# Optimization experiments

Measured on AMD Instinct MI355X. Metric: run time of the kernel, lower is better.

Reference implementation:

```python
import jax, jax.numpy as jnp
import numpy as np

N_A = 3
N_CLS = 80
IGNORE_THRE = 0.6
EPS = 1e-7


def _pairwise_iou_cxcywh(a, b):
    # a: [..., M, 4], b: [..., N, 4] in (cx, cy, w, h) -> IoU [..., M, N]
    a_xy, a_wh = a[..., :, None, :2], a[..., :, None, 2:4]
    b_xy, b_wh = b[..., None, :, :2], b[..., None, :, 2:4]
    tl = jnp.maximum(a_xy - a_wh * 0.5, b_xy - b_wh * 0.5)
    br = jnp.minimum(a_xy + a_wh * 0.5, b_xy + b_wh * 0.5)
    inter = jnp.prod(jnp.clip(br - tl, 0.0), axis=-1)
    area_a = a_wh[..., 0] * a_wh[..., 1]
    area_b = b_wh[..., 0] * b_wh[..., 1]
    return inter / jnp.maximum(area_a + area_b - inter, 1e-16)


def _bce(p, t):
    p = jnp.clip(p, EPS, 1.0 - EPS)
    return -(t * jnp.log(p) + (1.0 - t) * jnp.log(1.0 - p))


def _yolo_loss(raw, labels, anchors_all, anchor_indices, img_size):
    nB = raw.shape[0]
    nG = raw.shape[2]
    nCH = 5 + N_CLS
    K = labels.shape[1]
    sg = jax.lax.stop_gradient

    # decode raw: (B, A*CH, G, G) -> (B, A, G, G, CH)
    raw = jnp.transpose(raw.reshape(nB, N_A, nCH, nG, nG), (0, 1, 3, 4, 2))
    xy_offset = jax.nn.sigmoid(raw[..., 0:2])            # (B,A,G,G,2)
    wh_scale = raw[..., 2:4]                             # (B,A,G,G,2)
    conf = jax.nn.sigmoid(raw[..., 4])                   # (B,A,G,G)
    classes = jax.nn.sigmoid(raw[..., 5:])               # (B,A,G,G,ncls)

    anchors = anchors_all[anchor_indices]                # (3,2), pixels
    g = jnp.arange(nG, dtype=raw.dtype)
    xs = g[None, None, None, :]
    ys = g[None, None, :, None]

    # detached decoded predictions, normalized to [0,1]
    px = (sg(xy_offset[..., 0]) + xs) / nG
    py = (sg(xy_offset[..., 1]) + ys) / nG
    pw = jnp.minimum(jnp.exp(sg(wh_scale[..., 0])) * anchors[:, 0][None, :, None, None] / img_size, 1.0)
    ph = jnp.minimum(jnp.exp(sg(wh_scale[..., 1])) * anchors[:, 1][None, :, None, None] / img_size, 1.0)
    pred_boxes = jnp.stack([px, py, pw, ph], axis=-1).reshape(nB, -1, 4)  # (B, A*G*G, 4)

    # labels: (B, K, 5) = [cls, xc, yc, w, h]; targets are constants
    labels = sg(labels)
    nlabel = jnp.sum(jnp.sum(labels, axis=2) > 0, axis=1)                 # (B,)
    valid_k = jnp.arange(K)[None, :] < nlabel[:, None]                    # (B,K)
    tcls = labels[..., 0].astype(jnp.int32)
    tx = labels[..., 1] * nG
    ty = labels[..., 2] * nG
    tw = labels[..., 3]
    th = labels[..., 4]
    ti = tx.astype(jnp.int32)
    tj = ty.astype(jnp.int32)

    # anchor matching on centered (0,0,w,h) boxes against all 9 anchors
    anch00 = jnp.concatenate([jnp.zeros_like(anchors_all), anchors_all / img_size], axis=1)  # (9,4)
    gt00 = jnp.stack([jnp.zeros_like(tw), jnp.zeros_like(tw), tw, th], axis=-1)              # (B,K,4)
    a_ious = _pairwise_iou_cxcywh(gt00, anch00[None])                                        # (B,K,9)
    best_n_all = jnp.argmax(a_ious, axis=-1)                                                 # (B,K)
    valid_anchor = jnp.any(best_n_all[..., None] == anchor_indices[None, None, :], axis=-1)
    valid = valid_k & valid_anchor                                                           # (B,K)
    best_n = best_n_all % N_A

    # ignore mask: preds whose best IoU against any (valid) gt exceeds threshold
    gt_boxes = jnp.stack([tx / nG, ty / nG, tw, th], axis=-1) * valid_k[..., None].astype(raw.dtype)
    pred_ious = _pairwise_iou_cxcywh(pred_boxes, gt_boxes)               # (B, A*G*G, K)
    ignore = (jnp.max(pred_ious, axis=-1) > IGNORE_THRE).reshape(nB, N_A, nG, nG)
    penalty_mask = ~ignore

    # scatter gt assignments; invalid rows dropped via OOB batch index
    b_idx = jnp.broadcast_to(jnp.arange(nB)[:, None], (nB, K))
    b_s = jnp.where(valid, b_idx, nB)

    obj_mask = jnp.zeros((nB, N_A, nG, nG), dtype=bool).at[b_s, best_n, tj, ti].set(True, mode='drop')
    penalty_mask = penalty_mask.at[b_s, best_n, tj, ti].set(True, mode='drop')

    naw = anchors / img_size                                             # (3,2)
    tgt_vals = jnp.stack([
        tx - jnp.floor(tx),
        ty - jnp.floor(ty),
        jnp.log(tw / naw[best_n, 0] + 1e-16),
        jnp.log(th / naw[best_n, 1] + 1e-16),
    ], axis=-1)                                                          # (B,K,4)
    target4 = jnp.zeros((nB, N_A, nG, nG, 4), raw.dtype).at[b_s, best_n, tj, ti].set(tgt_vals, mode='drop')
    tgt_scale = jnp.zeros((nB, N_A, nG, nG), raw.dtype).at[b_s, best_n, tj, ti].set(
        jnp.sqrt(2.0 - tw * th), mode='drop')
    tcls_oh = jnp.zeros((nB, N_A, nG, nG, N_CLS), raw.dtype).at[b_s, best_n, tj, ti, tcls].set(1.0, mode='drop')

    obj_f = obj_mask.astype(raw.dtype)
    pen_f = penalty_mask.astype(raw.dtype)
    w2 = tgt_scale * tgt_scale                                           # (B,A,G,G)

    loss_xy = jnp.sum(obj_f[..., None] * w2[..., None] * _bce(xy_offset, target4[..., 0:2]))
    loss_wh = jnp.sum(obj_f[..., None] * w2[..., None] * jnp.square(wh_scale - target4[..., 2:4]))
    loss_obj = jnp.sum(pen_f * _bce(conf, obj_f))
    loss_cls = jnp.sum(obj_f[..., None] * _bce(classes, tcls_oh))
    return loss_xy + 0.5 * loss_wh + loss_obj + loss_cls


def setup_inputs() -> dict:
    key = jax.random.key(0)
    k1, k2, k3, k4 = jax.random.split(key, 4)
    nB, K, nG = 16, 50, 76
    raw = jax.random.normal(k1, (nB, N_A * (5 + N_CLS), nG, nG), jnp.float32) * 0.5
    cls = jax.random.randint(k2, (nB, K), 0, N_CLS).astype(jnp.float32)
    xy = jax.random.uniform(k3, (nB, K, 2), jnp.float32, 0.02, 0.98)
    wh = jax.random.uniform(k4, (nB, K, 2), jnp.float32, 0.02, 0.4)
    labels = jnp.concatenate([cls[..., None], xy, wh], axis=-1)
    # make per-image label counts < K (rows of zeros are "no label")
    labels = labels * (jnp.arange(K) < 40).astype(jnp.float32)[None, :, None]
    anchors_all = jnp.array([[10, 13], [16, 30], [33, 23], [30, 61], [62, 45],
                             [59, 119], [116, 90], [156, 198], [373, 326]], jnp.float32)
    anchor_indices = jnp.array([0, 1, 2], jnp.int32)
    return {"raw": raw, "labels": labels, "anchors_all": anchors_all,
            "anchor_indices": anchor_indices, "img_size": 608}


def reference(raw, labels, anchors_all, anchor_indices, img_size):
    return _yolo_loss(raw, labels, anchors_all, anchor_indices, img_size)
```

## Files before the change

### kernel.cpp

```cpp
#include <hip/hip_runtime.h>
#include <math.h>

#define NB   16
#define KL   50
#define NG   76
#define NA   3
#define NCLS 80
#define NCH  85
#define GG   (NG*NG)
#define CELLS (NA*GG)
#define LOSS_BX ((CELLS + 255) / 256)
#define NPART (LOSS_BX * NB)

__device__ __forceinline__ float softplusf(float x) {
    float t = __expf(-fabsf(x));
    return fmaxf(x, 0.0f) + __logf(1.0f + t);
}

__global__ __launch_bounds__(64) void yolo_prep(
    const float* __restrict__ labels,
    const float* __restrict__ anchors_all,
    const int*   __restrict__ anchor_indices,
    const int*   __restrict__ img_size_p,
    int*    __restrict__ meta_ws,
    float4* __restrict__ box_ws,
    float*  __restrict__ c_ws,
    float*  __restrict__ tgt_ws,
    float*  __restrict__ w2_ws,
    int*    __restrict__ tc_ws)
{
    const int b = blockIdx.x;
    const int k = threadIdx.x;
    const float img = (float)img_size_p[0];

    int has = 0;
    float cls = 0.f, tx = 0.f, ty = 0.f, tw = 0.f, th = 0.f;
    if (k < KL) {
        const float* L = labels + ((size_t)b * KL + k) * 5;
        cls = L[0];
        float lx = L[1], ly = L[2];
        tw = L[3]; th = L[4];
        has = ((cls + lx + ly + tw + th) > 0.0f) ? 1 : 0;
        tx = lx * (float)NG;
        ty = ly * (float)NG;
    }
    unsigned long long bal = __ballot(has);
    int nlabel = __popcll(bal);
    if (k >= KL) return;

    int valid_k = (k < nlabel) ? 1 : 0;

    float best = -1.0f; int bestn = 0;
    float area_t = tw * th;
    for (int n = 0; n < 9; ++n) {
        float aw = anchors_all[2 * n + 0] / img;
        float ah = anchors_all[2 * n + 1] / img;
        float inter = fmaxf(fminf(tw, aw), 0.0f) * fmaxf(fminf(th, ah), 0.0f);
        float iou = inter / fmaxf(area_t + aw * ah - inter, 1e-16f);
        if (iou > best) { best = iou; bestn = n; }
    }
    int va = 0;
    for (int t = 0; t < 3; ++t) va |= (bestn == anchor_indices[t]) ? 1 : 0;
    int bn = bestn % NA;
    int ti = (int)tx, tj = (int)ty;
    int valid = valid_k && va && (ti >= 0) && (ti < NG) && (tj >= 0) && (tj < NG);

    const size_t idx = (size_t)b * KL + k;
    meta_ws[idx] = valid ? (bn * GG + tj * NG + ti) : -1;

    float vkf = valid_k ? 1.0f : 0.0f;
    float gx = (tx / (float)NG) * vkf;
    float gy = (ty / (float)NG) * vkf;
    float gw = tw * vkf;
    float gh = th * vkf;
    box_ws[idx] = make_float4(gx - 0.5f * gw, gy - 0.5f * gh,
                              gx + 0.5f * gw, gy + 0.5f * gh);
    c_ws[idx] = 0.375f * (gw * gh);

    float naw = anchors_all[anchor_indices[bn] * 2 + 0] / img;
    float nah = anchors_all[anchor_indices[bn] * 2 + 1] / img;
    float* T = tgt_ws + idx * 4;
    T[0] = tx - floorf(tx);
    T[1] = ty - floorf(ty);
    T[2] = logf(tw / naw + 1e-16f);
    T[3] = logf(th / nah + 1e-16f);
    w2_ws[idx] = 2.0f - tw * th;
    tc_ws[idx] = (int)cls;
}

__global__ __launch_bounds__(256) void yolo_loss(
    const float* __restrict__ raw,
    const float* __restrict__ anchors_all,
    const int*   __restrict__ anchor_indices,
    const int*   __restrict__ img_size_p,
    const int*   __restrict__ meta_ws,
    const float4* __restrict__ box_ws,
    const float* __restrict__ c_ws,
    const float* __restrict__ tgt_ws,
    const float* __restrict__ w2_ws,
    const int*   __restrict__ tc_ws,
    float* __restrict__ partials)
{
    const int b = blockIdx.y;
    const int c0 = blockIdx.x * 256 + threadIdx.x;
    const bool live = c0 < CELLS;
    const int c = live ? c0 : 0;

    const int a = c / GG;
    const int r = c - a * GG;
    const int j = r / NG;
    const int i = r - j * NG;
    const float img = (float)img_size_p[0];
    const float* R = raw + ((size_t)(b * NA + a) * NCH) * GG + r;

    float rx = R[0],        ry = R[GG];
    float rw = R[2 * GG],   rh = R[3 * GG];
    float rc = R[4 * GG];

    float sx = __builtin_amdgcn_rcpf(1.0f + __expf(-rx));
    float sy = __builtin_amdgcn_rcpf(1.0f + __expf(-ry));

    int ai = anchor_indices[a];
    float aw = anchors_all[2 * ai + 0] / img;
    float ah = anchors_all[2 * ai + 1] / img;

    float px = (sx + (float)i) * (1.0f / (float)NG);
    float py = (sy + (float)j) * (1.0f / (float)NG);
    float pw = fminf(__expf(rw) * aw, 1.0f);
    float ph = fminf(__expf(rh) * ah, 1.0f);

    float tA = 0.375f * (pw * ph);
    float ax0 = px - 0.5f * pw, ax1 = px + 0.5f * pw;
    float ay0 = py - 0.5f * ph, ay1 = py + 0.5f * ph;

    const float4* __restrict__ Gbox  = box_ws  + (size_t)b * KL;
    const float*  __restrict__ Gc    = c_ws    + (size_t)b * KL;
    const int*    __restrict__ Gmeta = meta_ws + (size_t)b * KL;

    float margin = -1.0f;
    int kobj = -1;
    #pragma unroll 10
    for (int k = 0; k < KL; ++k) {
        float4 g = Gbox[k];
        float cB = Gc[k];
        int   mk = Gmeta[k];
        float iw = fminf(ax1, g.z) - fmaxf(ax0, g.x);
        float ih = fminf(ay1, g.w) - fmaxf(ay0, g.y);
        float inter = fmaxf(iw, 0.0f) * fmaxf(ih, 0.0f);
        margin = fmaxf(margin, inter - cB);
        kobj = (mk == c) ? k : kobj;
    }
    bool ignore = margin > tA;
    bool obj = (kobj >= 0) && live;

    float loss = 0.0f;
    if (obj || !ignore)
        loss = softplusf(rc) - (obj ? rc : 0.0f);

    if (obj) {
        size_t kb = (size_t)b * KL + kobj;
        float w2 = w2_ws[kb];
        float t0 = tgt_ws[4 * kb + 0], t1 = tgt_ws[4 * kb + 1];
        float t2 = tgt_ws[4 * kb + 2], t3 = tgt_ws[4 * kb + 3];
        loss += w2 * ((softplusf(rx) - t0 * rx) + (softplusf(ry) - t1 * ry));
        float dw = rw - t2, dh = rh - t3;
        loss += 0.5f * w2 * (dw * dw + dh * dh);
        int tc = tc_ws[kb];
        float cl = 0.0f;
        #pragma unroll 8
        for (int cc = 0; cc < NCLS; ++cc) {
            float z = R[(5 + cc) * GG];
            cl += softplusf(z);
            if (cc == tc) cl -= z;
        }
        loss += cl;
    }
    if (!live) loss = 0.0f;

    for (int off = 32; off > 0; off >>= 1)
        loss += __shfl_down(loss, off, 64);
    __shared__ float s_red[4];
    if ((threadIdx.x & 63) == 0) s_red[threadIdx.x >> 6] = loss;
    __syncthreads();
    if (threadIdx.x == 0)
        partials[(size_t)blockIdx.y * gridDim.x + blockIdx.x] =
            s_red[0] + s_red[1] + s_red[2] + s_red[3];
}

__global__ __launch_bounds__(256) void yolo_finalize(
    const float* __restrict__ partials, float* __restrict__ out)
{
    float s = 0.0f;
    for (int i = threadIdx.x; i < NPART; i += 256) s += partials[i];
    for (int off = 32; off > 0; off >>= 1)
        s += __shfl_down(s, off, 64);
    __shared__ float red[4];
    if ((threadIdx.x & 63) == 0) red[threadIdx.x >> 6] = s;
    __syncthreads();
    if (threadIdx.x == 0) out[0] = red[0] + red[1] + red[2] + red[3];
}

extern "C" void kernel_launch(void* const* d_in, const int* in_sizes, int n_in,
                              void* d_out, int out_size, void* d_ws, size_t ws_size,
                              hipStream_t stream) {
    const float* raw            = (const float*)d_in[0];
    const float* labels         = (const float*)d_in[1];
    const float* anchors_all    = (const float*)d_in[2];
    const int*   anchor_indices = (const int*)d_in[3];
    const int*   img_size_p     = (const int*)d_in[4];
    float* out = (float*)d_out;

    char* ws = (char*)d_ws;
    float4* box_ws  = (float4*)ws;  ws += sizeof(float4) * NB * KL;
    float*  tgt_ws  = (float*)ws;   ws += sizeof(float)  * NB * KL * 4;
    float*  c_ws    = (float*)ws;   ws += sizeof(float)  * NB * KL;
    float*  w2_ws   = (float*)ws;   ws += sizeof(float)  * NB * KL;
    int*    meta_ws = (int*)ws;     ws += sizeof(int)    * NB * KL;
    int*    tc_ws   = (int*)ws;     ws += sizeof(int)    * NB * KL;
    float*  partials= (float*)ws;   ws += sizeof(float)  * NPART;

    yolo_prep<<<NB, 64, 0, stream>>>(labels, anchors_all, anchor_indices,
                                     img_size_p, meta_ws, box_ws, c_ws,
                                     tgt_ws, w2_ws, tc_ws);

    dim3 grid(LOSS_BX, NB);
    yolo_loss<<<grid, 256, 0, stream>>>(raw, anchors_all, anchor_indices,
                                        img_size_p, meta_ws, box_ws, c_ws,
                                        tgt_ws, w2_ws, tc_ws, partials);

    yolo_finalize<<<1, 256, 0, stream>>>(partials, out);
}
```

Baseline: 146.2 us.

## Fuse label preprocessing into loss kernel using shared memory per block

Removes the separate prep kernel launch. Each loss block now recomputes the per-image label targets, boxes and match indices in its first wavefront and keeps them in LDS, so the inner 50-label loop reads shared memory instead of global workspace. This saves a launch and a global round trip, but every block repeats the small label computation and the other wavefronts wait at a barrier. Divisions by the image size become reciprocal multiplies, and logf becomes __logf.

```diff
diff --git a/kernel.cpp b/kernel.cpp
--- a/kernel.cpp
+++ b/kernel.cpp
@@ -17,91 +17,81 @@
     return fmaxf(x, 0.0f) + __logf(1.0f + t);
 }
 
-__global__ __launch_bounds__(64) void yolo_prep(
+__global__ __launch_bounds__(256) void yolo_fused(
+    const float* __restrict__ raw,
     const float* __restrict__ labels,
     const float* __restrict__ anchors_all,
     const int*   __restrict__ anchor_indices,
     const int*   __restrict__ img_size_p,
-    int*    __restrict__ meta_ws,
-    float4* __restrict__ box_ws,
-    float*  __restrict__ c_ws,
-    float*  __restrict__ tgt_ws,
-    float*  __restrict__ w2_ws,
-    int*    __restrict__ tc_ws)
-{
-    const int b = blockIdx.x;
-    const int k = threadIdx.x;
-    const float img = (float)img_size_p[0];
-
-    int has = 0;
-    float cls = 0.f, tx = 0.f, ty = 0.f, tw = 0.f, th = 0.f;
-    if (k < KL) {
-        const float* L = labels + ((size_t)b * KL + k) * 5;
-        cls = L[0];
-        float lx = L[1], ly = L[2];
-        tw = L[3]; th = L[4];
-        has = ((cls + lx + ly + tw + th) > 0.0f) ? 1 : 0;
-        tx = lx * (float)NG;
-        ty = ly * (float)NG;
-    }
-    unsigned long long bal = __ballot(has);
-    int nlabel = __popcll(bal);
-    if (k >= KL) return;
-
-    int valid_k = (k < nlabel) ? 1 : 0;
-
-    float best = -1.0f; int bestn = 0;
-    float area_t = tw * th;
-    for (int n = 0; n < 9; ++n) {
-        float aw = anchors_all[2 * n + 0] / img;
-        float ah = anchors_all[2 * n + 1] / img;
-        float inter = fmaxf(fminf(tw, aw), 0.0f) * fmaxf(fminf(th, ah), 0.0f);
-        float iou = inter / fmaxf(area_t + aw * ah - inter, 1e-16f);
-        if (iou > best) { best = iou; bestn = n; }
-    }
-    int va = 0;
-    for (int t = 0; t < 3; ++t) va |= (bestn == anchor_indices[t]) ? 1 : 0;
-    int bn = bestn % NA;
-    int ti = (int)tx, tj = (int)ty;
-    int valid = valid_k && va && (ti >= 0) && (ti < NG) && (tj >= 0) && (tj < NG);
-
-    const size_t idx = (size_t)b * KL + k;
-    meta_ws[idx] = valid ? (bn * GG + tj * NG + ti) : -1;
-
-    float vkf = valid_k ? 1.0f : 0.0f;
-    float gx = (tx / (float)NG) * vkf;
-    float gy = (ty / (float)NG) * vkf;
-    float gw = tw * vkf;
-    float gh = th * vkf;
-    box_ws[idx] = make_float4(gx - 0.5f * gw, gy - 0.5f * gh,
-                              gx + 0.5f * gw, gy + 0.5f * gh);
-    c_ws[idx] = 0.375f * (gw * gh);
-
-    float naw = anchors_all[anchor_indices[bn] * 2 + 0] / img;
-    float nah = anchors_all[anchor_indices[bn] * 2 + 1] / img;
-    float* T = tgt_ws + idx * 4;
-    T[0] = tx - floorf(tx);
-    T[1] = ty - floorf(ty);
-    T[2] = logf(tw / naw + 1e-16f);
-    T[3] = logf(th / nah + 1e-16f);
-    w2_ws[idx] = 2.0f - tw * th;
-    tc_ws[idx] = (int)cls;
-}
-
-__global__ __launch_bounds__(256) void yolo_loss(
-    const float* __restrict__ raw,
-    const float* __restrict__ anchors_all,
-    const int*   __restrict__ anchor_indices,
-    const int*   __restrict__ img_size_p,
-    const int*   __restrict__ meta_ws,
-    const float4* __restrict__ box_ws,
-    const float* __restrict__ c_ws,
-    const float* __restrict__ tgt_ws,
-    const float* __restrict__ w2_ws,
-    const int*   __restrict__ tc_ws,
     float* __restrict__ partials)
 {
     const int b = blockIdx.y;
+
+    __shared__ float4 s_box[KL];
+    __shared__ float  s_c[KL];
+    __shared__ int    s_meta[KL];
+    __shared__ float  s_tgt[KL][4];
+    __shared__ float  s_w2[KL];
+    __shared__ int    s_tc[KL];
+    __shared__ float  s_red[4];
+
+    const float img = (float)img_size_p[0];
+    const float inv_img = __builtin_amdgcn_rcpf(img);
+
+    if (threadIdx.x < 64) {
+        const int k = threadIdx.x;
+        int has = 0;
+        float cls = 0.f, tx = 0.f, ty = 0.f, tw = 0.f, th = 0.f;
+        if (k < KL) {
+            const float* L = labels + ((size_t)b * KL + k) * 5;
+            cls = L[0];
+            tw = L[3]; th = L[4];
+            has = ((cls + L[1] + L[2] + tw + th) > 0.0f) ? 1 : 0;
+            tx = L[1] * (float)NG;
+            ty = L[2] * (float)NG;
+        }
+        unsigned long long bal = __ballot(has);
+        int nlabel = __popcll(bal);
+
+        if (k < KL) {
+            int valid_k = (k < nlabel) ? 1 : 0;
+
+            float best = -1.0f; int bestn = 0;
+            float area_t = tw * th;
+            for (int n = 0; n < 9; ++n) {
+                float aw = anchors_all[2 * n + 0] * inv_img;
+                float ah = anchors_all[2 * n + 1] * inv_img;
+                float inter = fmaxf(fminf(tw, aw), 0.0f) * fmaxf(fminf(th, ah), 0.0f);
+                float iou = inter / fmaxf(area_t + aw * ah - inter, 1e-16f);
+                if (iou > best) { best = iou; bestn = n; }
+            }
+            int va = 0;
+            for (int t = 0; t < 3; ++t) va |= (bestn == anchor_indices[t]) ? 1 : 0;
+            int bn = bestn % NA;
+            int ti = (int)tx, tj = (int)ty;
+            int valid = valid_k && va && (ti >= 0) && (ti < NG) && (tj >= 0) && (tj < NG);
+            s_meta[k] = valid ? (bn * GG + tj * NG + ti) : -1;
+
+            float vkf = valid_k ? 1.0f : 0.0f;
+            float gx = tx * (1.0f / (float)NG) * vkf;
+            float gy = ty * (1.0f / (float)NG) * vkf;
+            float gw = tw * vkf, gh = th * vkf;
+            s_box[k] = make_float4(gx - 0.5f * gw, gy - 0.5f * gh,
+                                   gx + 0.5f * gw, gy + 0.5f * gh);
+            s_c[k] = 0.375f * (gw * gh);
+
+            float naw = anchors_all[anchor_indices[bn] * 2 + 0] * inv_img;
+            float nah = anchors_all[anchor_indices[bn] * 2 + 1] * inv_img;
+            s_tgt[k][0] = tx - floorf(tx);
+            s_tgt[k][1] = ty - floorf(ty);
+            s_tgt[k][2] = __logf(tw / naw + 1e-16f);
+            s_tgt[k][3] = __logf(th / nah + 1e-16f);
+            s_w2[k] = 2.0f - tw * th;
+            s_tc[k] = (int)cls;
+        }
+    }
+    __syncthreads();
+
     const int c0 = blockIdx.x * 256 + threadIdx.x;
     const bool live = c0 < CELLS;
     const int c = live ? c0 : 0;
@@ -110,19 +100,18 @@
     const int r = c - a * GG;
     const int j = r / NG;
     const int i = r - j * NG;
-    const float img = (float)img_size_p[0];
     const float* R = raw + ((size_t)(b * NA + a) * NCH) * GG + r;
 
-    float rx = R[0],        ry = R[GG];
-    float rw = R[2 * GG],   rh = R[3 * GG];
+    float rx = R[0],      ry = R[GG];
+    float rw = R[2 * GG], rh = R[3 * GG];
     float rc = R[4 * GG];
 
     float sx = __builtin_amdgcn_rcpf(1.0f + __expf(-rx));
     float sy = __builtin_amdgcn_rcpf(1.0f + __expf(-ry));
 
     int ai = anchor_indices[a];
-    float aw = anchors_all[2 * ai + 0] / img;
-    float ah = anchors_all[2 * ai + 1] / img;
+    float aw = anchors_all[2 * ai + 0] * inv_img;
+    float ah = anchors_all[2 * ai + 1] * inv_img;
 
     float px = (sx + (float)i) * (1.0f / (float)NG);
     float py = (sy + (float)j) * (1.0f / (float)NG);
@@ -133,22 +122,16 @@
     float ax0 = px - 0.5f * pw, ax1 = px + 0.5f * pw;
     float ay0 = py - 0.5f * ph, ay1 = py + 0.5f * ph;
 
-    const float4* __restrict__ Gbox  = box_ws  + (size_t)b * KL;
-    const float*  __restrict__ Gc    = c_ws    + (size_t)b * KL;
-    const int*    __restrict__ Gmeta = meta_ws + (size_t)b * KL;
-
     float margin = -1.0f;
     int kobj = -1;
     #pragma unroll 10
     for (int k = 0; k < KL; ++k) {
-        float4 g = Gbox[k];
-        float cB = Gc[k];
-        int   mk = Gmeta[k];
+        float4 g = s_box[k];
         float iw = fminf(ax1, g.z) - fmaxf(ax0, g.x);
         float ih = fminf(ay1, g.w) - fmaxf(ay0, g.y);
         float inter = fmaxf(iw, 0.0f) * fmaxf(ih, 0.0f);
-        margin = fmaxf(margin, inter - cB);
-        kobj = (mk == c) ? k : kobj;
+        margin = fmaxf(margin, inter - s_c[k]);
+        kobj = (s_meta[k] == c) ? k : kobj;
     }
     bool ignore = margin > tA;
     bool obj = (kobj >= 0) && live;
@@ -158,14 +141,13 @@
         loss = softplusf(rc) - (obj ? rc : 0.0f);
 
     if (obj) {
-        size_t kb = (size_t)b * KL + kobj;
-        float w2 = w2_ws[kb];
-        float t0 = tgt_ws[4 * kb + 0], t1 = tgt_ws[4 * kb + 1];
-        float t2 = tgt_ws[4 * kb + 2], t3 = tgt_ws[4 * kb + 3];
+        float w2 = s_w2[kobj];
+        float t0 = s_tgt[kobj][0], t1 = s_tgt[kobj][1];
+        float t2 = s_tgt[kobj][2], t3 = s_tgt[kobj][3];
         loss += w2 * ((softplusf(rx) - t0 * rx) + (softplusf(ry) - t1 * ry));
         float dw = rw - t2, dh = rh - t3;
         loss += 0.5f * w2 * (dw * dw + dh * dh);
-        int tc = tc_ws[kb];
+        int tc = s_tc[kobj];
         float cl = 0.0f;
         #pragma unroll 8
         for (int cc = 0; cc < NCLS; ++cc) {
@@ -179,7 +161,6 @@
 
     for (int off = 32; off > 0; off >>= 1)
         loss += __shfl_down(loss, off, 64);
-    __shared__ float s_red[4];
     if ((threadIdx.x & 63) == 0) s_red[threadIdx.x >> 6] = loss;
     __syncthreads();
     if (threadIdx.x == 0)
@@ -210,23 +191,10 @@
     const int*   img_size_p     = (const int*)d_in[4];
     float* out = (float*)d_out;
 
-    char* ws = (char*)d_ws;
-    float4* box_ws  = (float4*)ws;  ws += sizeof(float4) * NB * KL;
-    float*  tgt_ws  = (float*)ws;   ws += sizeof(float)  * NB * KL * 4;
-    float*  c_ws    = (float*)ws;   ws += sizeof(float)  * NB * KL;
-    float*  w2_ws   = (float*)ws;   ws += sizeof(float)  * NB * KL;
-    int*    meta_ws = (int*)ws;     ws += sizeof(int)    * NB * KL;
-    int*    tc_ws   = (int*)ws;     ws += sizeof(int)    * NB * KL;
-    float*  partials= (float*)ws;   ws += sizeof(float)  * NPART;
-
-    yolo_prep<<<NB, 64, 0, stream>>>(labels, anchors_all, anchor_indices,
-                                     img_size_p, meta_ws, box_ws, c_ws,
-                                     tgt_ws, w2_ws, tc_ws);
+    float* partials = (float*)d_ws;
 
     dim3 grid(LOSS_BX, NB);
-    yolo_loss<<<grid, 256, 0, stream>>>(raw, anchors_all, anchor_indices,
-                                        img_size_p, meta_ws, box_ws, c_ws,
-                                        tgt_ws, w2_ws, tc_ws, partials);
-
+    yolo_fused<<<grid, 256, 0, stream>>>(raw, labels, anchors_all,
+                                         anchor_indices, img_size_p, partials);
     yolo_finalize<<<1, 256, 0, stream>>>(partials, out);
 }
```

Measured after the change: 142.5 us. 2.5% less time.
